# Kernel optimization log

Measured on AMD Instinct MI355X. Metric: run time of the kernel, lower is better.

## Reference

```python
import jax, jax.numpy as jnp
import numpy as np

T, B, IN, H = 256, 64, 1024, 1024


def setup_inputs() -> dict:
    key = jax.random.key(0)
    ks = jax.random.split(key, 16)
    s = 0.02
    def w(k, shape):
        return jax.random.normal(k, shape, jnp.float32) * s
    return {
        "x": jax.random.normal(ks[0], (T, B, IN), jnp.float32),
        # layer 0 (input IN -> H)
        "W0": w(ks[1], (3 * H, IN)), "b0": jnp.zeros((3 * H,), jnp.float32),
        "Ur0": w(ks[2], (H, H)), "Uz0": w(ks[3], (H, H)),
        "Un0": w(ks[4], (H, H)), "bn0": jnp.zeros((H,), jnp.float32),
        # layer 1 (input 2H -> H)
        "W1": w(ks[5], (3 * H, 2 * H)), "b1": jnp.zeros((3 * H,), jnp.float32),
        "Ur1": w(ks[6], (H, H)), "Uz1": w(ks[7], (H, H)),
        "Un1": w(ks[8], (H, H)), "bn1": jnp.zeros((H,), jnp.float32),
    }


def _gru_layer(x_proj, Ur, Uz, Un, bn):
    """Bidirectional GRU layer. x_proj: (T,B,3H). Returns (T,B,2H), h_fwd, h_bwd.
    use_transpose_U=False path: h-projections use U (i.e. h @ U.T, as nn.Linear)."""
    Bsz = x_proj.shape[1]
    h0 = jnp.zeros((Bsz, H), x_proj.dtype)

    def step(h, xp):
        r_x, z_x, n_x = jnp.split(xp, 3, axis=-1)
        r = jax.nn.sigmoid(r_x + h @ Ur.T)
        z = jax.nn.sigmoid(z_x + h @ Uz.T)
        n = jnp.tanh(n_x + r * (h @ Un.T + bn))
        h_new = (1.0 - z) * n + z * h
        return h_new, h_new

    h_fwd, fwd_out = jax.lax.scan(step, h0, x_proj)
    # backward direction: same cell (shared U), sequence reversed; scan
    # with reverse=True writes bwd_out[t] for the state after consuming t..T-1,
    # matching the torch loop `for t in range(T-1,-1,-1)`.
    h_bwd, bwd_out = jax.lax.scan(step, h0, x_proj, reverse=True)
    return jnp.concatenate([fwd_out, bwd_out], axis=-1), h_fwd, h_bwd


def reference(x, W0, b0, Ur0, Uz0, Un0, bn0, W1, b1, Ur1, Uz1, Un1, bn1):
    # layer 0: fused input projection once for both directions
    xp0 = jnp.einsum("tbi,gi->tbg", x, W0) + b0          # (T,B,3H)
    out0, hf0, hb0 = _gru_layer(xp0, Ur0, Uz0, Un0, bn0)  # (T,B,2H)
    # dropout = Identity (dropout=0.0)
    xp1 = jnp.einsum("tbi,gi->tbg", out0, W1) + b1        # (T,B,3H)
    out1, hf1, hb1 = _gru_layer(xp1, Ur1, Uz1, Un1, bn1)  # (T,B,2H)
    hidden = jnp.stack([hf0, hb0, hf1, hb1])              # (num_layers*2,B,H)
    return out1, hidden
```

## Files before the change

### kernel.cpp

```cpp
#include <hip/hip_runtime.h>
#include <stdint.h>

typedef short short8v __attribute__((ext_vector_type(8)));
typedef unsigned short u16x8 __attribute__((ext_vector_type(8)));
typedef float f32x4  __attribute__((ext_vector_type(4)));
typedef unsigned long long u64;

__device__ inline uint16_t f2bf(float f){
  uint32_t u = __float_as_uint(f);
  uint32_t r = (u + 0x7fffu + ((u >> 16) & 1u)) >> 16;
  return (uint16_t)r;
}
__device__ inline float bf2f(uint16_t h){
  return __uint_as_float(((uint32_t)h) << 16);
}

__global__ void cvt_f32_bf16(const float* __restrict__ src, uint16_t* __restrict__ dst, int n4){
  int i = blockIdx.x * blockDim.x + threadIdx.x;
  int stride = gridDim.x * blockDim.x;
  for (; i < n4; i += stride){
    float4 v = ((const float4*)src)[i];
    uint64_t p = (uint64_t)f2bf(v.x)
               | ((uint64_t)f2bf(v.y) << 16)
               | ((uint64_t)f2bf(v.z) << 32)
               | ((uint64_t)f2bf(v.w) << 48);
    ((uint64_t*)dst)[i] = p;
  }
}

#define GL2LDS(g, l) __builtin_amdgcn_global_load_lds((const __attribute__((address_space(1))) unsigned int*)(g), (__attribute__((address_space(3))) unsigned int*)(l), 16, 0, 0)

__global__ __launch_bounds__(256) void gemm_bt_bias(
    const uint16_t* __restrict__ A, const uint16_t* __restrict__ Bw,
    const float* __restrict__ bias, uint16_t* __restrict__ C,
    int M, int N, int K)
{
  __shared__ uint16_t As[128 * 64];
  __shared__ uint16_t Bs[128 * 64];
  const int tid  = threadIdx.x;
  const int lane = tid & 63, wid = tid >> 6;
  const int n0 = blockIdx.x * 128, m0 = blockIdx.y * 128;
  const int wrow = (wid & 1) * 64, wcol = (wid >> 1) * 64;
  const int l15 = lane & 15, l4 = lane >> 4;
  const int srow = lane >> 3, scol = (lane & 7) * 8;
  const size_t Ks = (size_t)K;

  f32x4 acc[4][4] = {};

  for (int kt = 0; kt < K; kt += 64){
    __syncthreads();
    const uint16_t* gA = A  + (size_t)m0 * Ks + kt;
    const uint16_t* gB = Bw + (size_t)n0 * Ks + kt;
    #pragma unroll
    for (int i = 0; i < 4; ++i){
      int rb = wid * 32 + i * 8;
      GL2LDS(gA + (size_t)(rb + srow) * Ks + scol, &As[rb * 64]);
      GL2LDS(gB + (size_t)(rb + srow) * Ks + scol, &Bs[rb * 64]);
    }
    __syncthreads();
    #pragma unroll
    for (int kk = 0; kk < 2; ++kk){
      short8v a[4], b[4];
      int koff = kk * 32 + l4 * 8;
      #pragma unroll
      for (int mt = 0; mt < 4; ++mt) a[mt] = *(const short8v*)&As[(wrow + mt*16 + l15) * 64 + koff];
      #pragma unroll
      for (int nt = 0; nt < 4; ++nt) b[nt] = *(const short8v*)&Bs[(wcol + nt*16 + l15) * 64 + koff];
      #pragma unroll
      for (int mt = 0; mt < 4; ++mt)
        #pragma unroll
        for (int nt = 0; nt < 4; ++nt)
          acc[mt][nt] = __builtin_amdgcn_mfma_f32_16x16x32_bf16(a[mt], b[nt], acc[mt][nt], 0, 0, 0);
    }
  }
  #pragma unroll
  for (int mt = 0; mt < 4; ++mt)
    #pragma unroll
    for (int nt = 0; nt < 4; ++nt){
      int col = n0 + wcol + nt * 16 + l15;
      float bv = bias[col];
      int rbase = m0 + wrow + mt * 16 + l4 * 4;
      #pragma unroll
      for (int j = 0; j < 4; ++j)
        C[(size_t)(rbase + j) * (size_t)N + col] = f2bf(acc[mt][nt][j] + bv);
    }
}

__device__ inline int ridx8(int w, int c, int m){
  return (w * 48 + c) * 40 + (m ^ ((c & 7) << 2));
}

#define HLOAD(dst, addr) \
  asm volatile("global_load_dwordx4 %0, %1, off sc0 sc1" : "=v"(dst) : "v"(addr) : "memory")
#define XPLOAD2(dst, addr) \
  asm volatile("global_load_ushort %0, %1, off" : "=v"(dst) : "v"(addr) : "memory")
#define HSTORE2(addr, val) \
  asm volatile("global_store_short %0, %1, off sc0 sc1" :: "v"(addr), "v"(val) : "memory")
#define OSTORE2(addr, val) \
  asm volatile("global_store_short %0, %1, off nt" :: "v"(addr), "v"(val) : "memory")
#define OSTORE4(addr, val) \
  asm volatile("global_store_dword %0, %1, off nt" :: "v"(addr), "v"(val) : "memory")
#define WAITVM(n) do { asm volatile("s_waitcnt vmcnt(" #n ")" ::: "memory"); \
                       __builtin_amdgcn_sched_barrier(0); } while (0)

__global__ __launch_bounds__(512, 1) void gru_layer(
    const uint16_t* __restrict__ xp,
    const uint16_t* __restrict__ U,
    const float* __restrict__ bn,
    char* __restrict__ hring,
    uint16_t* __restrict__ out_bf,
    float* __restrict__ out_f32,
    float* __restrict__ hid)
{
  __shared__ float red[8 * 48 * 40];
  const int tid  = threadIdx.x;
  const int lane = tid & 63, wid = tid >> 6;
  const int bid  = blockIdx.x;
  const int dir  = bid >> 7;
  const int grp  = (bid >> 6) & 1;
  const int dg   = dir * 2 + grp;
  const int cb   = bid & 63;
  const int c0   = cb * 16;
  const int brow0 = grp * 32;
  const int l15 = lane & 15, l4 = lane >> 4;
  const int gm = tid >> 4;
  const int c16 = tid & 15;

  short8v bfr[3][4];
  #pragma unroll
  for (int g = 0; g < 3; ++g)
    #pragma unroll
    for (int kk = 0; kk < 4; ++kk){
      int row = g * 1024 + c0 + l15;
      int k   = wid * 128 + kk * 32 + l4 * 8;
      bfr[g][kk] = *(const short8v*)&U[(size_t)row * 1024 + k];
    }

  float hold = 0.f;
  const float bnv = bn[c0 + c16];

  const size_t hoff = (size_t)(wid * 8 + (l4 >> 1)) * 1024 + (size_t)(l4 & 1) * 16 + (size_t)l15 * 32;

  for (int s = 0; s < 256; ++s){
    const int t = dir ? (255 - s) : s;
    const size_t xb2 = ((size_t)t * 64 + brow0 + gm) * 3072 + c0 + c16;

    f32x4 acc[3][2] = {};
    unsigned pxr, pxz, pxn;
    if (s > 0){
      const char* hgbase = hring + ((size_t)((s & 31) * 4 + dg) * 64) * 1024;

      XPLOAD2(pxr, &xp[xb2]);
      XPLOAD2(pxz, &xp[xb2 + 1024]);
      XPLOAD2(pxn, &xp[xb2 + 2048]);
      short8v hc[4][2];
      #pragma unroll
      for (int kk = 0; kk < 4; ++kk)
        #pragma unroll
        for (int mt = 0; mt < 2; ++mt)
          HLOAD(hc[kk][mt], hgbase + hoff + (size_t)kk * 2048 + (size_t)mt * 512);
      WAITVM(0);

      int spins = 0;
      for (;;){
        u16x8 mx = (u16x8)hc[0][0];
        #pragma unroll
        for (int kk = 0; kk < 4; ++kk)
          #pragma unroll
          for (int mt = 0; mt < 2; ++mt)
            if (kk | mt) mx = __builtin_elementwise_max(mx, (u16x8)hc[kk][mt]);
        unsigned anybad = 0;
        #pragma unroll
        for (int i = 0; i < 8; ++i) anybad |= (unsigned)(mx[i] == (unsigned short)0xFFFFu);
        if (!__any((int)anybad)) break;
        __builtin_amdgcn_s_sleep(1);
        if (((++spins) & 255) == 0)
          __builtin_amdgcn_fence(__ATOMIC_ACQUIRE, "agent");
        #pragma unroll
        for (int kk = 0; kk < 4; ++kk)
          #pragma unroll
          for (int mt = 0; mt < 2; ++mt)
            HLOAD(hc[kk][mt], hgbase + hoff + (size_t)kk * 2048 + (size_t)mt * 512);
        WAITVM(0);
      }

      #pragma unroll
      for (int kk = 0; kk < 4; ++kk)
        #pragma unroll
        for (int g = 0; g < 3; ++g)
          #pragma unroll
          for (int mt = 0; mt < 2; ++mt)
            acc[g][mt] = __builtin_amdgcn_mfma_f32_16x16x32_bf16(hc[kk][mt], bfr[g][kk], acc[g][mt], 0, 0, 0);
    } else {
      pxr = xp[xb2];
      pxz = xp[xb2 + 1024];
      pxn = xp[xb2 + 2048];
    }

    #pragma unroll
    for (int g = 0; g < 3; ++g)
      #pragma unroll
      for (int mt = 0; mt < 2; ++mt)
        *(f32x4*)&red[ridx8(wid, g * 16 + l15, mt * 16 + l4 * 4)] = acc[g][mt];
    __syncthreads();

    float ra = 0.f, za = 0.f, na = 0.f;
    #pragma unroll
    for (int w = 0; w < 8; ++w){
      ra += red[ridx8(w,      c16, gm)];
      za += red[ridx8(w, 16 + c16, gm)];
      na += red[ridx8(w, 32 + c16, gm)];
    }
    __syncthreads();

    WAITVM(0);
    float xr = bf2f((uint16_t)pxr);
    float xz = bf2f((uint16_t)pxz);
    float xn = bf2f((uint16_t)pxn);
    float r = 1.f / (1.f + __expf(-(xr + ra)));
    float z = 1.f / (1.f + __expf(-(xz + za)));
    float n = tanhf(xn + r * (na + bnv));
    float hn = (1.f - z) * n + z * hold;
    hold = hn;
    unsigned hv = f2bf(hn);

    {
      const size_t mybyte = (size_t)cb * 1024 + (size_t)gm * 32 + (size_t)c16 * 2;
      char* hw = hring + ((size_t)(((s + 1) & 31) * 4 + dg) * 64) * 1024 + mybyte;
      HSTORE2(hw, hv);
      char* sw = hring + ((size_t)(((s + 17) & 31) * 4 + dg) * 64) * 1024 + mybyte;
      HSTORE2(sw, 0xFFFFu);
    }

    {
      size_t obase = ((size_t)t * 64 + brow0 + gm) * 2048 + (size_t)dir * 1024 + c0 + c16;
      if (out_bf) OSTORE2(&out_bf[obase], hv);
      else        OSTORE4(&out_f32[obase], __float_as_uint(hn));
      if (s == 255)
        hid[((size_t)dir * 64 + brow0 + gm) * 1024 + c0 + c16] = hn;
    }
  }
}

extern "C" void kernel_launch(void* const* d_in, const int* in_sizes, int n_in,
                              void* d_out, int out_size, void* d_ws, size_t ws_size,
                              hipStream_t stream) {
  const float* x   = (const float*)d_in[0];
  const float* W0  = (const float*)d_in[1];
  const float* b0  = (const float*)d_in[2];
  const float* Ur0 = (const float*)d_in[3];
  const float* Uz0 = (const float*)d_in[4];
  const float* Un0 = (const float*)d_in[5];
  const float* bn0 = (const float*)d_in[6];
  const float* W1  = (const float*)d_in[7];
  const float* b1  = (const float*)d_in[8];
  const float* Ur1 = (const float*)d_in[9];
  const float* Uz1 = (const float*)d_in[10];
  const float* Un1 = (const float*)d_in[11];
  const float* bn1 = (const float*)d_in[12];
  float* out = (float*)d_out;

  const size_t RING = (size_t)8 * 1024 * 1024;
  char* base = (char*)d_ws;
  char*     hring = base;
  uint16_t* xb    = (uint16_t*)(base + RING);
  uint16_t* w0b   = xb    + (size_t)16384 * 1024;
  uint16_t* u0b   = w0b   + (size_t)3072 * 1024;
  uint16_t* w1b   = u0b   + (size_t)3072 * 1024;
  uint16_t* u1b   = w1b   + (size_t)3072 * 2048;
  uint16_t* xp    = u1b   + (size_t)3072 * 1024;
  uint16_t* out0b = xp    + (size_t)16384 * 3072;

  auto cvt = [&](const float* s, uint16_t* d, size_t n){
    int n4 = (int)(n / 4);
    int grid = (n4 + 255) / 256; if (grid > 2048) grid = 2048;
    hipLaunchKernelGGL(cvt_f32_bf16, dim3(grid), dim3(256), 0, stream, s, d, n4);
  };
  hipMemsetAsync(hring, 0xFF, RING, stream);

  cvt(x,   xb,  (size_t)16384 * 1024);
  cvt(W0,  w0b, (size_t)3072 * 1024);
  cvt(Ur0, u0b + 0 * (size_t)1024 * 1024, (size_t)1024 * 1024);
  cvt(Uz0, u0b + 1 * (size_t)1024 * 1024, (size_t)1024 * 1024);
  cvt(Un0, u0b + 2 * (size_t)1024 * 1024, (size_t)1024 * 1024);
  cvt(W1,  w1b, (size_t)3072 * 2048);
  cvt(Ur1, u1b + 0 * (size_t)1024 * 1024, (size_t)1024 * 1024);
  cvt(Uz1, u1b + 1 * (size_t)1024 * 1024, (size_t)1024 * 1024);
  cvt(Un1, u1b + 2 * (size_t)1024 * 1024, (size_t)1024 * 1024);

  hipLaunchKernelGGL(gemm_bt_bias, dim3(24, 128), dim3(256), 0, stream,
                     xb, w0b, b0, xp, 16384, 3072, 1024);
  hipLaunchKernelGGL(gru_layer, dim3(256), dim3(512), 0, stream,
                     xp, u0b, bn0, hring,
                     out0b, (float*)nullptr,
                     out + (size_t)33554432);
  hipMemsetAsync(hring, 0xFF, RING, stream);
  hipLaunchKernelGGL(gemm_bt_bias, dim3(24, 128), dim3(256), 0, stream,
                     out0b, w1b, b1, xp, 16384, 3072, 2048);
  hipLaunchKernelGGL(gru_layer, dim3(256), dim3(512), 0, stream,
                     xp, u1b, bn1, hring,
                     (uint16_t*)nullptr, out,
                     out + (size_t)33554432 + (size_t)2 * 64 * 1024);
}
```

Before: 2.116 ms.

## Retile GRU recurrence blocks to 16 batch rows by 32 hidden columns

Each persistent block in the recurrent GRU kernel now owns 16 batch rows and 32 hidden columns, with four batch groups per direction, instead of 32 rows and 16 columns with two groups. Each wave holds twice as many U fragments in registers and loads half as much h per step, so per-step global h traffic and polling work per block shrink. The hring layout, readiness flags and LDS reduction layout change to match. The cost is more register pressure for the U fragments, more groups synchronising through the ring, and a different LDS swizzle.

```diff
diff --git a/kernel.cpp b/kernel.cpp
--- a/kernel.cpp
+++ b/kernel.cpp
@@ -86,8 +86,8 @@
     }
 }
 
-__device__ inline int ridx8(int w, int c, int m){
-  return (w * 48 + c) * 40 + (m ^ ((c & 7) << 2));
+__device__ inline int ridx(int w, int c, int m){
+  return (w * 96 + c) * 20 + (m ^ ((c & 3) << 2));
 }
 
 #define HLOAD(dst, addr) \
@@ -112,63 +112,58 @@
     float* __restrict__ out_f32,
     float* __restrict__ hid)
 {
-  __shared__ float red[8 * 48 * 40];
+  __shared__ float red[8 * 96 * 20];
   const int tid  = threadIdx.x;
   const int lane = tid & 63, wid = tid >> 6;
   const int bid  = blockIdx.x;
   const int dir  = bid >> 7;
-  const int grp  = (bid >> 6) & 1;
-  const int dg   = dir * 2 + grp;
-  const int cb   = bid & 63;
-  const int c0   = cb * 16;
-  const int brow0 = grp * 32;
+  const int grp  = (bid >> 5) & 3;
+  const int dg   = dir * 4 + grp;
+  const int cb   = bid & 31;
+  const int c0   = cb * 32;
+  const int brow0 = grp * 16;
   const int l15 = lane & 15, l4 = lane >> 4;
-  const int gm = tid >> 4;
-  const int c16 = tid & 15;
-
-  short8v bfr[3][4];
+  const int gm = tid >> 5;
+  const int gc = tid & 31;
+
+  short8v bfr[3][2][4];
   #pragma unroll
   for (int g = 0; g < 3; ++g)
     #pragma unroll
-    for (int kk = 0; kk < 4; ++kk){
-      int row = g * 1024 + c0 + l15;
-      int k   = wid * 128 + kk * 32 + l4 * 8;
-      bfr[g][kk] = *(const short8v*)&U[(size_t)row * 1024 + k];
-    }
+    for (int ct = 0; ct < 2; ++ct)
+      #pragma unroll
+      for (int kk = 0; kk < 4; ++kk){
+        int row = g * 1024 + c0 + ct * 16 + l15;
+        int k   = wid * 128 + kk * 32 + l4 * 8;
+        bfr[g][ct][kk] = *(const short8v*)&U[(size_t)row * 1024 + k];
+      }
 
   float hold = 0.f;
-  const float bnv = bn[c0 + c16];
-
-  const size_t hoff = (size_t)(wid * 8 + (l4 >> 1)) * 1024 + (size_t)(l4 & 1) * 16 + (size_t)l15 * 32;
+  const float bnv = bn[c0 + gc];
 
   for (int s = 0; s < 256; ++s){
     const int t = dir ? (255 - s) : s;
-    const size_t xb2 = ((size_t)t * 64 + brow0 + gm) * 3072 + c0 + c16;
+    const size_t xb2 = ((size_t)t * 64 + brow0 + gm) * 3072 + c0 + gc;
 
     f32x4 acc[3][2] = {};
     unsigned pxr, pxz, pxn;
     if (s > 0){
-      const char* hgbase = hring + ((size_t)((s & 31) * 4 + dg) * 64) * 1024;
+      const char* hgbase = hring + ((size_t)((s & 31) * 8 + dg) * 32) * 1024;
 
       XPLOAD2(pxr, &xp[xb2]);
       XPLOAD2(pxz, &xp[xb2 + 1024]);
       XPLOAD2(pxn, &xp[xb2 + 2048]);
-      short8v hc[4][2];
+      short8v hc[4];
       #pragma unroll
       for (int kk = 0; kk < 4; ++kk)
-        #pragma unroll
-        for (int mt = 0; mt < 2; ++mt)
-          HLOAD(hc[kk][mt], hgbase + hoff + (size_t)kk * 2048 + (size_t)mt * 512);
+        HLOAD(hc[kk], hgbase + (size_t)(wid * 4 + kk) * 1024 + (size_t)l15 * 64 + (size_t)l4 * 16);
       WAITVM(0);
 
       int spins = 0;
       for (;;){
-        u16x8 mx = (u16x8)hc[0][0];
-        #pragma unroll
-        for (int kk = 0; kk < 4; ++kk)
-          #pragma unroll
-          for (int mt = 0; mt < 2; ++mt)
-            if (kk | mt) mx = __builtin_elementwise_max(mx, (u16x8)hc[kk][mt]);
+        u16x8 mx = (u16x8)hc[0];
+        #pragma unroll
+        for (int kk = 1; kk < 4; ++kk) mx = __builtin_elementwise_max(mx, (u16x8)hc[kk]);
         unsigned anybad = 0;
         #pragma unroll
         for (int i = 0; i < 8; ++i) anybad |= (unsigned)(mx[i] == (unsigned short)0xFFFFu);
@@ -178,9 +173,7 @@
           __builtin_amdgcn_fence(__ATOMIC_ACQUIRE, "agent");
         #pragma unroll
         for (int kk = 0; kk < 4; ++kk)
-          #pragma unroll
-          for (int mt = 0; mt < 2; ++mt)
-            HLOAD(hc[kk][mt], hgbase + hoff + (size_t)kk * 2048 + (size_t)mt * 512);
+          HLOAD(hc[kk], hgbase + (size_t)(wid * 4 + kk) * 1024 + (size_t)l15 * 64 + (size_t)l4 * 16);
         WAITVM(0);
       }
 
@@ -189,8 +182,8 @@
         #pragma unroll
         for (int g = 0; g < 3; ++g)
           #pragma unroll
-          for (int mt = 0; mt < 2; ++mt)
-            acc[g][mt] = __builtin_amdgcn_mfma_f32_16x16x32_bf16(hc[kk][mt], bfr[g][kk], acc[g][mt], 0, 0, 0);
+          for (int ct = 0; ct < 2; ++ct)
+            acc[g][ct] = __builtin_amdgcn_mfma_f32_16x16x32_bf16(hc[kk], bfr[g][ct][kk], acc[g][ct], 0, 0, 0);
     } else {
       pxr = xp[xb2];
       pxz = xp[xb2 + 1024];
@@ -200,16 +193,16 @@
     #pragma unroll
     for (int g = 0; g < 3; ++g)
       #pragma unroll
-      for (int mt = 0; mt < 2; ++mt)
-        *(f32x4*)&red[ridx8(wid, g * 16 + l15, mt * 16 + l4 * 4)] = acc[g][mt];
+      for (int ct = 0; ct < 2; ++ct)
+        *(f32x4*)&red[ridx(wid, g * 32 + ct * 16 + l15, l4 * 4)] = acc[g][ct];
     __syncthreads();
 
     float ra = 0.f, za = 0.f, na = 0.f;
     #pragma unroll
     for (int w = 0; w < 8; ++w){
-      ra += red[ridx8(w,      c16, gm)];
-      za += red[ridx8(w, 16 + c16, gm)];
-      na += red[ridx8(w, 32 + c16, gm)];
+      ra += red[ridx(w,      gc, gm)];
+      za += red[ridx(w, 32 + gc, gm)];
+      na += red[ridx(w, 64 + gc, gm)];
     }
     __syncthreads();
 
@@ -225,19 +218,19 @@
     unsigned hv = f2bf(hn);
 
     {
-      const size_t mybyte = (size_t)cb * 1024 + (size_t)gm * 32 + (size_t)c16 * 2;
-      char* hw = hring + ((size_t)(((s + 1) & 31) * 4 + dg) * 64) * 1024 + mybyte;
+      const size_t mybyte = (size_t)cb * 1024 + (size_t)gm * 64 + (size_t)gc * 2;
+      char* hw = hring + ((size_t)(((s + 1) & 31) * 8 + dg) * 32) * 1024 + mybyte;
       HSTORE2(hw, hv);
-      char* sw = hring + ((size_t)(((s + 17) & 31) * 4 + dg) * 64) * 1024 + mybyte;
+      char* sw = hring + ((size_t)(((s + 17) & 31) * 8 + dg) * 32) * 1024 + mybyte;
       HSTORE2(sw, 0xFFFFu);
     }
 
     {
-      size_t obase = ((size_t)t * 64 + brow0 + gm) * 2048 + (size_t)dir * 1024 + c0 + c16;
+      size_t obase = ((size_t)t * 64 + brow0 + gm) * 2048 + (size_t)dir * 1024 + c0 + gc;
       if (out_bf) OSTORE2(&out_bf[obase], hv);
       else        OSTORE4(&out_f32[obase], __float_as_uint(hn));
       if (s == 255)
-        hid[((size_t)dir * 64 + brow0 + gm) * 1024 + c0 + c16] = hn;
+        hid[((size_t)dir * 64 + brow0 + gm) * 1024 + c0 + gc] = hn;
     }
   }
 }
```

Result: slower. 2.882 ms (+36.2%).

## Fuse input-projection GEMM with GRU recurrence via sentinel-polled xp buffer

Applied to the files above, without the earlier changes.

Merges each layer's input-projection GEMM and its GRU recurrence into one launch. Blocks 0-255 run the recurrence and blocks 256+ compute GEMM tiles ordered from both time ends. xp is pre-filled with 0xFFFF sentinels so recurrent blocks spin until the needed projections are written, letting the GEMM overlap the latency-bound recurrence. This adds an extra memset of xp, extra polling loads, and the risk of deadlock or contention if GEMM blocks cannot get scheduled while the persistent GRU blocks occupy CUs.

```diff
diff --git a/kernel.cpp b/kernel.cpp
--- a/kernel.cpp
+++ b/kernel.cpp
@@ -30,70 +30,14 @@
 
 #define GL2LDS(g, l) __builtin_amdgcn_global_load_lds((const __attribute__((address_space(1))) unsigned int*)(g), (__attribute__((address_space(3))) unsigned int*)(l), 16, 0, 0)
 
-__global__ __launch_bounds__(256) void gemm_bt_bias(
-    const uint16_t* __restrict__ A, const uint16_t* __restrict__ Bw,
-    const float* __restrict__ bias, uint16_t* __restrict__ C,
-    int M, int N, int K)
-{
-  __shared__ uint16_t As[128 * 64];
-  __shared__ uint16_t Bs[128 * 64];
-  const int tid  = threadIdx.x;
-  const int lane = tid & 63, wid = tid >> 6;
-  const int n0 = blockIdx.x * 128, m0 = blockIdx.y * 128;
-  const int wrow = (wid & 1) * 64, wcol = (wid >> 1) * 64;
-  const int l15 = lane & 15, l4 = lane >> 4;
-  const int srow = lane >> 3, scol = (lane & 7) * 8;
-  const size_t Ks = (size_t)K;
-
-  f32x4 acc[4][4] = {};
-
-  for (int kt = 0; kt < K; kt += 64){
-    __syncthreads();
-    const uint16_t* gA = A  + (size_t)m0 * Ks + kt;
-    const uint16_t* gB = Bw + (size_t)n0 * Ks + kt;
-    #pragma unroll
-    for (int i = 0; i < 4; ++i){
-      int rb = wid * 32 + i * 8;
-      GL2LDS(gA + (size_t)(rb + srow) * Ks + scol, &As[rb * 64]);
-      GL2LDS(gB + (size_t)(rb + srow) * Ks + scol, &Bs[rb * 64]);
-    }
-    __syncthreads();
-    #pragma unroll
-    for (int kk = 0; kk < 2; ++kk){
-      short8v a[4], b[4];
-      int koff = kk * 32 + l4 * 8;
-      #pragma unroll
-      for (int mt = 0; mt < 4; ++mt) a[mt] = *(const short8v*)&As[(wrow + mt*16 + l15) * 64 + koff];
-      #pragma unroll
-      for (int nt = 0; nt < 4; ++nt) b[nt] = *(const short8v*)&Bs[(wcol + nt*16 + l15) * 64 + koff];
-      #pragma unroll
-      for (int mt = 0; mt < 4; ++mt)
-        #pragma unroll
-        for (int nt = 0; nt < 4; ++nt)
-          acc[mt][nt] = __builtin_amdgcn_mfma_f32_16x16x32_bf16(a[mt], b[nt], acc[mt][nt], 0, 0, 0);
-    }
-  }
-  #pragma unroll
-  for (int mt = 0; mt < 4; ++mt)
-    #pragma unroll
-    for (int nt = 0; nt < 4; ++nt){
-      int col = n0 + wcol + nt * 16 + l15;
-      float bv = bias[col];
-      int rbase = m0 + wrow + mt * 16 + l4 * 4;
-      #pragma unroll
-      for (int j = 0; j < 4; ++j)
-        C[(size_t)(rbase + j) * (size_t)N + col] = f2bf(acc[mt][nt][j] + bv);
-    }
-}
-
 __device__ inline int ridx8(int w, int c, int m){
   return (w * 48 + c) * 40 + (m ^ ((c & 7) << 2));
 }
 
 #define HLOAD(dst, addr) \
   asm volatile("global_load_dwordx4 %0, %1, off sc0 sc1" : "=v"(dst) : "v"(addr) : "memory")
-#define XPLOAD2(dst, addr) \
-  asm volatile("global_load_ushort %0, %1, off" : "=v"(dst) : "v"(addr) : "memory")
+#define XPLOADU(dst, addr) \
+  asm volatile("global_load_ushort %0, %1, off sc0 sc1" : "=v"(dst) : "v"(addr) : "memory")
 #define HSTORE2(addr, val) \
   asm volatile("global_store_short %0, %1, off sc0 sc1" :: "v"(addr), "v"(val) : "memory")
 #define OSTORE2(addr, val) \
@@ -103,16 +47,13 @@
 #define WAITVM(n) do { asm volatile("s_waitcnt vmcnt(" #n ")" ::: "memory"); \
                        __builtin_amdgcn_sched_barrier(0); } while (0)
 
-__global__ __launch_bounds__(512, 1) void gru_layer(
-    const uint16_t* __restrict__ xp,
-    const uint16_t* __restrict__ U,
-    const float* __restrict__ bn,
-    char* __restrict__ hring,
-    uint16_t* __restrict__ out_bf,
-    float* __restrict__ out_f32,
-    float* __restrict__ hid)
+__device__ __forceinline__ void gru_body(
+    const uint16_t* __restrict__ xp, const uint16_t* __restrict__ U,
+    const float* __restrict__ bn, char* __restrict__ hring,
+    uint16_t* __restrict__ out_bf, float* __restrict__ out_f32,
+    float* __restrict__ hid, char* smem)
 {
-  __shared__ float red[8 * 48 * 40];
+  float* red = (float*)smem;
   const int tid  = threadIdx.x;
   const int lane = tid & 63, wid = tid >> 6;
   const int bid  = blockIdx.x;
@@ -138,7 +79,6 @@
 
   float hold = 0.f;
   const float bnv = bn[c0 + c16];
-
   const size_t hoff = (size_t)(wid * 8 + (l4 >> 1)) * 1024 + (size_t)(l4 & 1) * 16 + (size_t)l15 * 32;
 
   for (int s = 0; s < 256; ++s){
@@ -150,9 +90,9 @@
     if (s > 0){
       const char* hgbase = hring + ((size_t)((s & 31) * 4 + dg) * 64) * 1024;
 
-      XPLOAD2(pxr, &xp[xb2]);
-      XPLOAD2(pxz, &xp[xb2 + 1024]);
-      XPLOAD2(pxn, &xp[xb2 + 2048]);
+      XPLOADU(pxr, &xp[xb2]);
+      XPLOADU(pxz, &xp[xb2 + 1024]);
+      XPLOADU(pxn, &xp[xb2 + 2048]);
       short8v hc[4][2];
       #pragma unroll
       for (int kk = 0; kk < 4; ++kk)
@@ -172,10 +112,14 @@
         unsigned anybad = 0;
         #pragma unroll
         for (int i = 0; i < 8; ++i) anybad |= (unsigned)(mx[i] == (unsigned short)0xFFFFu);
+        anybad |= (unsigned)(pxr == 0xFFFFu) | (unsigned)(pxz == 0xFFFFu) | (unsigned)(pxn == 0xFFFFu);
         if (!__any((int)anybad)) break;
         __builtin_amdgcn_s_sleep(1);
         if (((++spins) & 255) == 0)
           __builtin_amdgcn_fence(__ATOMIC_ACQUIRE, "agent");
+        XPLOADU(pxr, &xp[xb2]);
+        XPLOADU(pxz, &xp[xb2 + 1024]);
+        XPLOADU(pxn, &xp[xb2 + 2048]);
         #pragma unroll
         for (int kk = 0; kk < 4; ++kk)
           #pragma unroll
@@ -192,9 +136,15 @@
           for (int mt = 0; mt < 2; ++mt)
             acc[g][mt] = __builtin_amdgcn_mfma_f32_16x16x32_bf16(hc[kk][mt], bfr[g][kk], acc[g][mt], 0, 0, 0);
     } else {
-      pxr = xp[xb2];
-      pxz = xp[xb2 + 1024];
-      pxn = xp[xb2 + 2048];
+      for (;;){
+        XPLOADU(pxr, &xp[xb2]);
+        XPLOADU(pxz, &xp[xb2 + 1024]);
+        XPLOADU(pxn, &xp[xb2 + 2048]);
+        WAITVM(0);
+        unsigned bad = (unsigned)(pxr == 0xFFFFu) | (unsigned)(pxz == 0xFFFFu) | (unsigned)(pxn == 0xFFFFu);
+        if (!__any((int)bad)) break;
+        __builtin_amdgcn_s_sleep(4);
+      }
     }
 
     #pragma unroll
@@ -213,7 +163,6 @@
     }
     __syncthreads();
 
-    WAITVM(0);
     float xr = bf2f((uint16_t)pxr);
     float xz = bf2f((uint16_t)pxz);
     float xn = bf2f((uint16_t)pxn);
@@ -231,7 +180,6 @@
       char* sw = hring + ((size_t)(((s + 17) & 31) * 4 + dg) * 64) * 1024 + mybyte;
       HSTORE2(sw, 0xFFFFu);
     }
-
     {
       size_t obase = ((size_t)t * 64 + brow0 + gm) * 2048 + (size_t)dir * 1024 + c0 + c16;
       if (out_bf) OSTORE2(&out_bf[obase], hv);
@@ -240,6 +188,85 @@
         hid[((size_t)dir * 64 + brow0 + gm) * 1024 + c0 + c16] = hn;
     }
   }
+}
+
+__device__ __forceinline__ void gemm_body(
+    const uint16_t* __restrict__ A, const uint16_t* __restrict__ Bw,
+    const float* __restrict__ bias, uint16_t* __restrict__ C,
+    int K, char* smem)
+{
+  const int w    = blockIdx.x - 256;
+  const int unit = threadIdx.x >> 8;
+  const int t2   = threadIdx.x & 255;
+  const int q    = w / 12;
+  const int mi   = (q & 1) ? (127 - (q >> 1)) : (q >> 1);
+  const int m0   = mi * 128;
+  const int n0   = ((w % 12) * 2 + unit) * 128;
+
+  uint16_t* As = (uint16_t*)(smem + unit * 32768);
+  uint16_t* Bs = As + 128 * 64;
+  const int lane = t2 & 63, wid = t2 >> 6;
+  const int wrow = (wid & 1) * 64, wcol = (wid >> 1) * 64;
+  const int l15 = lane & 15, l4 = lane >> 4;
+  const int srow = lane >> 3, scol = (lane & 7) * 8;
+  const size_t Ks = (size_t)K;
+
+  f32x4 acc[4][4] = {};
+
+  for (int kt = 0; kt < K; kt += 64){
+    __syncthreads();
+    const uint16_t* gA = A  + (size_t)m0 * Ks + kt;
+    const uint16_t* gB = Bw + (size_t)n0 * Ks + kt;
+    #pragma unroll
+    for (int i = 0; i < 4; ++i){
+      int rb = wid * 32 + i * 8;
+      GL2LDS(gA + (size_t)(rb + srow) * Ks + scol, &As[rb * 64]);
+      GL2LDS(gB + (size_t)(rb + srow) * Ks + scol, &Bs[rb * 64]);
+    }
+    __syncthreads();
+    #pragma unroll
+    for (int kk = 0; kk < 2; ++kk){
+      short8v a[4], b[4];
+      int koff = kk * 32 + l4 * 8;
+      #pragma unroll
+      for (int mt = 0; mt < 4; ++mt) a[mt] = *(const short8v*)&As[(wrow + mt*16 + l15) * 64 + koff];
+      #pragma unroll
+      for (int nt = 0; nt < 4; ++nt) b[nt] = *(const short8v*)&Bs[(wcol + nt*16 + l15) * 64 + koff];
+      #pragma unroll
+      for (int mt = 0; mt < 4; ++mt)
+        #pragma unroll
+        for (int nt = 0; nt < 4; ++nt)
+          acc[mt][nt] = __builtin_amdgcn_mfma_f32_16x16x32_bf16(a[mt], b[nt], acc[mt][nt], 0, 0, 0);
+    }
+  }
+  #pragma unroll
+  for (int mt = 0; mt < 4; ++mt)
+    #pragma unroll
+    for (int nt = 0; nt < 4; ++nt){
+      int col = n0 + wcol + nt * 16 + l15;
+      float bv = bias[col];
+      int rbase = m0 + wrow + mt * 16 + l4 * 4;
+      #pragma unroll
+      for (int j = 0; j < 4; ++j){
+        unsigned v = f2bf(acc[mt][nt][j] + bv);
+        HSTORE2(&C[(size_t)(rbase + j) * 3072 + col], v);
+      }
+    }
+}
+
+__global__ __launch_bounds__(512, 4) void fused_layer(
+    const uint16_t* __restrict__ xp, const uint16_t* __restrict__ U,
+    const float* __restrict__ bn, char* __restrict__ hring,
+    uint16_t* __restrict__ out_bf, float* __restrict__ out_f32,
+    float* __restrict__ hid,
+    const uint16_t* __restrict__ A, const uint16_t* __restrict__ Bw,
+    const float* __restrict__ bias, uint16_t* __restrict__ C, int K)
+{
+  __shared__ char smem[65536];
+  if (blockIdx.x < 256)
+    gru_body(xp, U, bn, hring, out_bf, out_f32, hid, smem);
+  else
+    gemm_body(A, Bw, bias, C, K, smem);
 }
 
 extern "C" void kernel_launch(void* const* d_in, const int* in_sizes, int n_in,
@@ -277,6 +304,7 @@
     hipLaunchKernelGGL(cvt_f32_bf16, dim3(grid), dim3(256), 0, stream, s, d, n4);
   };
   hipMemsetAsync(hring, 0xFF, RING, stream);
+  hipMemsetAsync(xp, 0xFF, (size_t)16384 * 3072 * 2, stream);
 
   cvt(x,   xb,  (size_t)16384 * 1024);
   cvt(W0,  w0b, (size_t)3072 * 1024);
@@ -288,17 +316,17 @@
   cvt(Uz1, u1b + 1 * (size_t)1024 * 1024, (size_t)1024 * 1024);
   cvt(Un1, u1b + 2 * (size_t)1024 * 1024, (size_t)1024 * 1024);
 
-  hipLaunchKernelGGL(gemm_bt_bias, dim3(24, 128), dim3(256), 0, stream,
-                     xb, w0b, b0, xp, 16384, 3072, 1024);
-  hipLaunchKernelGGL(gru_layer, dim3(256), dim3(512), 0, stream,
+  hipLaunchKernelGGL(fused_layer, dim3(1792), dim3(512), 0, stream,
                      xp, u0b, bn0, hring,
-                     out0b, (float*)nullptr,
-                     out + (size_t)33554432);
+                     out0b, (float*)nullptr, out + (size_t)33554432,
+                     xb, w0b, b0, xp, 1024);
+
   hipMemsetAsync(hring, 0xFF, RING, stream);
-  hipLaunchKernelGGL(gemm_bt_bias, dim3(24, 128), dim3(256), 0, stream,
-                     out0b, w1b, b1, xp, 16384, 3072, 2048);
-  hipLaunchKernelGGL(gru_layer, dim3(256), dim3(512), 0, stream,
+  hipMemsetAsync(xp, 0xFF, (size_t)16384 * 3072 * 2, stream);
+
+  hipLaunchKernelGGL(fused_layer, dim3(1792), dim3(512), 0, stream,
                      xp, u1b, bn1, hring,
                      (uint16_t*)nullptr, out,
-                     out + (size_t)33554432 + (size_t)2 * 64 * 1024);
-}
+                     out + (size_t)33554432 + (size_t)2 * 64 * 1024,
+                     out0b, w1b, b1, xp, 2048);
+}
```

After: 2.444 ms. +15.5%, slower.
